# Kernel optimization log

Measured on AMD Instinct MI355X. Metric: run time of the kernel, lower is better.

Reference implementation:

```python
import jax, jax.numpy as jnp
import numpy as np

B = 8192
I = 1024
H = 1024


def _xavier(key, out_dim, in_dim):
    limit = float(np.sqrt(6.0 / (in_dim + out_dim)))
    return jax.random.uniform(key, (out_dim, in_dim), jnp.float32, -limit, limit)


def setup_inputs() -> dict:
    key = jax.random.key(0)
    ks = jax.random.split(key, 16)
    inp = {
        "x": jax.random.normal(ks[0], (B, I), jnp.float32),
        "h_prev": jax.random.normal(ks[1], (B, H), jnp.float32),
        "c_prev": jax.random.normal(ks[2], (B, H), jnp.float32),
        # input->hidden weights (hidden_size, input_size), hidden->hidden (hidden_size, hidden_size)
        "Wxi": _xavier(ks[3], H, I), "Whi": _xavier(ks[4], H, H),
        "Wxf": _xavier(ks[5], H, I), "Whf": _xavier(ks[6], H, H),
        "Wxc": _xavier(ks[7], H, I), "Whc": _xavier(ks[8], H, H),
        "Wxo": _xavier(ks[9], H, I), "Who": _xavier(ks[10], H, H),
        "bxi": jnp.zeros((H,), jnp.float32), "bhi": jnp.zeros((H,), jnp.float32),
        # forget-gate biases initialized to ones per _init_weights
        "bxf": jnp.ones((H,), jnp.float32), "bhf": jnp.ones((H,), jnp.float32),
        "bxc": jnp.zeros((H,), jnp.float32), "bhc": jnp.zeros((H,), jnp.float32),
        "bxo": jnp.zeros((H,), jnp.float32), "bho": jnp.zeros((H,), jnp.float32),
    }
    return inp


def reference(x, h_prev, c_prev,
              Wxi, Whi, Wxf, Whf, Wxc, Whc, Wxo, Who,
              bxi, bhi, bxf, bhf, bxc, bhc, bxo, bho):
    # Fuse the 8 small linears into two GEMMs: stack along the output (gate) axis.
    Wx = jnp.concatenate([Wxi, Wxf, Wxc, Wxo], axis=0)   # (4H, I)
    Wh = jnp.concatenate([Whi, Whf, Whc, Who], axis=0)   # (4H, H)
    bx = jnp.concatenate([bxi, bxf, bxc, bxo], axis=0)    # (4H,)
    bh = jnp.concatenate([bhi, bhf, bhc, bho], axis=0)    # (4H,)
    gates = x @ Wx.T + h_prev @ Wh.T + (bx + bh)           # (B, 4H)
    zi, zf, zc, zo = jnp.split(gates, 4, axis=1)
    i = jax.nn.sigmoid(zi)
    f = jax.nn.sigmoid(zf)
    g = jnp.tanh(zc)
    o = jax.nn.sigmoid(zo)
    c_new = f * c_prev + i * g
    h_new = o * jnp.tanh(c_new)
    return (h_new, c_new)
```

## Files before the change

### kernel.cpp

```cpp
#include <hip/hip_runtime.h>
#include <hip/hip_bf16.h>
#include <stdint.h>


#define B_DIM 8192
#define I_DIM 1024
#define H_DIM 1024
#define K_DIM 2048
#define N_DIM 4096
#define NKT   32

typedef short bf16x8 __attribute__((ext_vector_type(8)));
typedef float f32x4 __attribute__((ext_vector_type(4)));

__device__ __forceinline__ unsigned short f2bf(float f) {
  unsigned int u = __float_as_uint(f);
  u += 0x7FFFu + ((u >> 16) & 1u);
  return (unsigned short)(u >> 16);
}

__global__ void pack_AB_kernel(const float* __restrict__ x, const float* __restrict__ h,
                               const float* __restrict__ Wxi, const float* __restrict__ Whi,
                               const float* __restrict__ Wxf, const float* __restrict__ Whf,
                               const float* __restrict__ Wxc, const float* __restrict__ Whc,
                               const float* __restrict__ Wxo, const float* __restrict__ Who,
                               unsigned short* __restrict__ outA,
                               unsigned short* __restrict__ outB) {
  const int totalA = B_DIM * K_DIM / 8;
  const int total  = totalA + N_DIM * K_DIM / 8;
  for (int idx = blockIdx.x * blockDim.x + threadIdx.x; idx < total;
       idx += gridDim.x * blockDim.x) {
    const float* src;
    unsigned short* dst;
    if (idx < totalA) {
      int row = idx >> 8;
      int col = (idx & 255) * 8;
      src = (col < I_DIM) ? (x + (size_t)row * I_DIM + col)
                          : (h + (size_t)row * H_DIM + (col - I_DIM));
      dst = outA + (size_t)idx * 8;
    } else {
      int u2 = idx - totalA;
      int r = u2 >> 8;
      int k = (u2 & 255) * 8;
      int g = (r >> 4) & 3;
      int hh = ((r >> 6) << 4) | (r & 15);
      src = (k < I_DIM)
          ? ((g == 0 ? Wxi : g == 1 ? Wxf : g == 2 ? Wxc : Wxo) + (size_t)hh * I_DIM + k)
          : ((g == 0 ? Whi : g == 1 ? Whf : g == 2 ? Whc : Who) + (size_t)hh * H_DIM + (k - I_DIM));
      dst = outB + (size_t)u2 * 8;
    }
    const float4* s4 = (const float4*)src;
    float4 v0 = s4[0], v1 = s4[1];
    bf16x8 o;
    o[0] = f2bf(v0.x); o[1] = f2bf(v0.y); o[2] = f2bf(v0.z); o[3] = f2bf(v0.w);
    o[4] = f2bf(v1.x); o[5] = f2bf(v1.y); o[6] = f2bf(v1.z); o[7] = f2bf(v1.w);
    *(bf16x8*)dst = o;
  }
}


#define STAGE(gptr, slotoff, ktile) do {                                          \
    int _ktc = (ktile) < NKT ? (ktile) : (NKT - 1);                               \
    const unsigned short* _g = (gptr) + (size_t)_ktc * 64;                        \
    __builtin_amdgcn_global_load_lds(                                             \
        (const __attribute__((address_space(1))) void*)_g,                        \
        (__attribute__((address_space(3))) void*)(lds + (slotoff) + wid * 1024),  \
        16, 0, 0);                                                                \
    __builtin_amdgcn_global_load_lds(                                             \
        (const __attribute__((address_space(1))) void*)(_g + (size_t)64 * K_DIM), \
        (__attribute__((address_space(3))) void*)(lds + (slotoff) + 8192 + wid * 1024), \
        16, 0, 0);                                                                \
  } while (0)

#define MFMAP(MH, AR, BR)                                                         \
  _Pragma("unroll") for (int mf = 0; mf < 4; ++mf)                                \
  _Pragma("unroll") for (int nn = 0; nn < 4; ++nn)                                \
    acc[(MH)*4 + mf][nn] = __builtin_amdgcn_mfma_f32_16x16x32_bf16(               \
        AR[mf], BR[nn], acc[(MH)*4 + mf][nn], 0, 0, 0)

#define RD_AQ(DST, MH, KOFF, BO)                                                  \
  _Pragma("unroll") for (int mf = 0; mf < 4; ++mf)                                \
    DST[mf] = *(const bf16x8*)(ldsAr + (BO) + (MH)*8192 + mf * 2048 + (KOFF));

#define RD_BH(DST, KOFF, BO)                                                      \
  _Pragma("unroll") for (int nn = 0; nn < 4; ++nn)                                \
    DST[nn] = *(const bf16x8*)(ldsBr + (BO) + nn * 2048 + (KOFF));

#define KTILE(BUF, KT) do {                                                       \
    const int _bo = (BUF) * 32768;                                                \
    const int _bo1 = ((BUF) ^ 1) * 32768;                                         \
                                                                          \
    __builtin_amdgcn_s_setprio(1);                                                \
    MFMAP(0, AQa, BHa);                                                           \
    __builtin_amdgcn_s_setprio(0);                                                \
    RD_AQ(AQb, 1, rd0, _bo);                                                      \
    __builtin_amdgcn_s_barrier();                                                 \
                                                                          \
    __builtin_amdgcn_s_setprio(1);                                                \
    MFMAP(1, AQb, BHa);                                                           \
    __builtin_amdgcn_s_setprio(0);                                                \
    RD_BH(BHb, rd1, _bo);                                                         \
    RD_AQ(AQa, 0, rd1, _bo);                                                      \
    __builtin_amdgcn_s_barrier();                                                 \
                                                                          \
    __builtin_amdgcn_s_setprio(1);                                                \
    MFMAP(0, AQa, BHb);                                                           \
    __builtin_amdgcn_s_setprio(0);                                                \
    RD_AQ(AQb, 1, rd1, _bo);                                                      \
    STAGE(gB0p, 65536 + _bo, (KT) + 2);                                           \
    STAGE(gB1p, 65536 + _bo + 16384, (KT) + 2);                                   \
    asm volatile("s_waitcnt vmcnt(4)" ::: "memory");                              \
    __builtin_amdgcn_s_barrier();                                                 \
                                                                          \
    __builtin_amdgcn_s_setprio(1);                                                \
    MFMAP(1, AQb, BHb);                                                           \
    __builtin_amdgcn_s_setprio(0);                                                \
    RD_AQ(AQa, 0, rd0, _bo1);                                                     \
    RD_BH(BHa, rd0, _bo1);                                                        \
    STAGE(gA0p, _bo, (KT) + 2);                                                   \
    STAGE(gA1p, _bo + 16384, (KT) + 2);                                           \
    __builtin_amdgcn_s_barrier();                                                 \
  } while (0)

__launch_bounds__(512, 2)
__global__ void lstm_gemm_kernel(const unsigned short* __restrict__ A,
                                 const unsigned short* __restrict__ Bp,
                                 const float* __restrict__ c_prev,
                                 const float* __restrict__ bxi, const float* __restrict__ bhi,
                                 const float* __restrict__ bxf, const float* __restrict__ bhf,
                                 const float* __restrict__ bxc, const float* __restrict__ bhc,
                                 const float* __restrict__ bxo, const float* __restrict__ bho,
                                 float* __restrict__ out) {
  __shared__ __align__(16) char lds[131072];

  const int nwg = gridDim.x;
  int bid = blockIdx.x;
  int q = nwg >> 3;
  int wg = (bid & 7) * q + (bid >> 3);
  int bm = wg >> 4;
  int bn = wg & 15;

  int tid = threadIdx.x;
  int lane = tid & 63;
  int wid = tid >> 6;
  int wm = wid >> 2;
  int wn = wid & 3;

  int srow = lane >> 3;
  int schunk = (lane & 7) ^ srow;
  const unsigned short* gA0p = A  + (size_t)(bm * 256 + wid * 8 + srow) * K_DIM + schunk * 8;
  const unsigned short* gA1p = gA0p + (size_t)128 * K_DIM;
  const unsigned short* gB0p = Bp + (size_t)(bn * 256 + wid * 8 + srow) * K_DIM + schunk * 8;
  const unsigned short* gB1p = gB0p + (size_t)128 * K_DIM;

  int c15 = lane & 15;
  int kl = lane >> 4;
  const char* ldsAr = lds + wm * 16384 + c15 * 128;
  const char* ldsBr = lds + 65536 + (wn >> 1) * 16384 + ((wn & 1) * 64 + c15) * 128;
  int rd0 = ((kl) ^ (lane & 7)) << 4;
  int rd1 = ((4 | kl) ^ (lane & 7)) << 4;

  f32x4 acc[8][4];
  f32x4 zero = {0.f, 0.f, 0.f, 0.f};
#pragma unroll
  for (int m = 0; m < 8; ++m)
#pragma unroll
    for (int n = 0; n < 4; ++n) acc[m][n] = zero;

  bf16x8 AQa[4], AQb[4];
  bf16x8 BHa[4], BHb[4];

  STAGE(gA0p, 0, 0);
  STAGE(gA1p, 16384, 0);
  STAGE(gB0p, 65536, 0);
  STAGE(gB1p, 65536 + 16384, 0);
  STAGE(gA0p, 32768, 1);
  STAGE(gA1p, 32768 + 16384, 1);
  STAGE(gB0p, 65536 + 32768, 1);
  STAGE(gB1p, 65536 + 32768 + 16384, 1);
  asm volatile("s_waitcnt vmcnt(8)" ::: "memory");
  __builtin_amdgcn_s_barrier();
  RD_AQ(AQa, 0, rd0, 0);
  RD_BH(BHa, rd0, 0);

#pragma unroll 1
  for (int kt = 0; kt < NKT; kt += 2) {
    KTILE(0, kt);
    KTILE(1, kt + 1);
  }

  int h = (bn * 4 + wn) * 16 + c15;
  float bi = bxi[h] + bhi[h];
  float bf_ = bxf[h] + bhf[h];
  float bc = bxc[h] + bhc[h];
  float bo = bxo[h] + bho[h];
  int row0 = bm * 256 + wm * 128 + kl * 4;
#pragma unroll
  for (int mi = 0; mi < 8; ++mi) {
#pragma unroll
    for (int j = 0; j < 4; ++j) {
      int r = row0 + mi * 16 + j;
      size_t off = (size_t)r * H_DIM + h;
      float zi = acc[mi][0][j] + bi;
      float zf = acc[mi][1][j] + bf_;
      float zc = acc[mi][2][j] + bc;
      float zo = acc[mi][3][j] + bo;
      float ig = 1.f / (1.f + __expf(-zi));
      float fg = 1.f / (1.f + __expf(-zf));
      float e2 = __expf(-2.f * zc);
      float gg = (1.f - e2) / (1.f + e2);
      float og = 1.f / (1.f + __expf(-zo));
      float cp = c_prev[off];
      float cn = fg * cp + ig * gg;
      float e2c = __expf(-2.f * cn);
      float th = (1.f - e2c) / (1.f + e2c);
      out[off] = og * th;
      out[(size_t)B_DIM * H_DIM + off] = cn;
    }
  }
}

extern "C" void kernel_launch(void* const* d_in, const int* in_sizes, int n_in,
                              void* d_out, int out_size, void* d_ws, size_t ws_size,
                              hipStream_t stream) {
  const float* x      = (const float*)d_in[0];
  const float* h_prev = (const float*)d_in[1];
  const float* c_prev = (const float*)d_in[2];
  const float* Wxi = (const float*)d_in[3];
  const float* Whi = (const float*)d_in[4];
  const float* Wxf = (const float*)d_in[5];
  const float* Whf = (const float*)d_in[6];
  const float* Wxc = (const float*)d_in[7];
  const float* Whc = (const float*)d_in[8];
  const float* Wxo = (const float*)d_in[9];
  const float* Who = (const float*)d_in[10];
  const float* bxi = (const float*)d_in[11];
  const float* bhi = (const float*)d_in[12];
  const float* bxf = (const float*)d_in[13];
  const float* bhf = (const float*)d_in[14];
  const float* bxc = (const float*)d_in[15];
  const float* bhc = (const float*)d_in[16];
  const float* bxo = (const float*)d_in[17];
  const float* bho = (const float*)d_in[18];

  unsigned short* Abf = (unsigned short*)d_ws;
  unsigned short* Bbf = (unsigned short*)((char*)d_ws + (size_t)B_DIM * K_DIM * 2);

  pack_AB_kernel<<<2048, 256, 0, stream>>>(x, h_prev,
      Wxi, Whi, Wxf, Whf, Wxc, Whc, Wxo, Who, Abf, Bbf);
  lstm_gemm_kernel<<<512, 512, 0, stream>>>(Abf, Bbf, c_prev,
      bxi, bhi, bxf, bhf, bxc, bhc, bxo, bho, (float*)d_out);
}
```

Baseline: 152.1 us.

## Shrink GEMM workgroup tile to 256x128 with K=32 stages and 4 waves

Reworks the bf16 MFMA GEMM from 512-thread workgroups with 256x256 tiles and K-step 64 into 256-thread workgroups with 256x128 tiles and K-step 32. That cuts LDS use from 128KB to 48KB, doubles the grid to 1024 blocks, and uses a new swizzle and a simpler two-phase double-buffered schedule with sched_barriers. The goal is better occupancy and load balance across CUs and simpler LDS reads. In exchange, arithmetic intensity per tile drops, B-matrix reuse is halved, and twice as many K iterations add barrier overhead.

Result: slower. 178.3 us (+17.3%).

```diff
diff --git a/kernel.cpp b/kernel.cpp
--- a/kernel.cpp
+++ b/kernel.cpp
@@ -8,7 +8,7 @@
 #define H_DIM 1024
 #define K_DIM 2048
 #define N_DIM 4096
-#define NKT   32
+#define NKT   64
 
 typedef short bf16x8 __attribute__((ext_vector_type(8)));
 typedef float f32x4 __attribute__((ext_vector_type(4)));
@@ -59,17 +59,22 @@
 }
 
 
-#define STAGE(gptr, slotoff, ktile) do {                                          \
-    int _ktc = (ktile) < NKT ? (ktile) : (NKT - 1);                               \
-    const unsigned short* _g = (gptr) + (size_t)_ktc * 64;                        \
-    __builtin_amdgcn_global_load_lds(                                             \
-        (const __attribute__((address_space(1))) void*)_g,                        \
-        (__attribute__((address_space(3))) void*)(lds + (slotoff) + wid * 1024),  \
-        16, 0, 0);                                                                \
-    __builtin_amdgcn_global_load_lds(                                             \
-        (const __attribute__((address_space(1))) void*)(_g + (size_t)64 * K_DIM), \
-        (__attribute__((address_space(3))) void*)(lds + (slotoff) + 8192 + wid * 1024), \
-        16, 0, 0);                                                                \
+#define STAGE_A(BUF, KT) do {                                                     \
+    int _ktc = (KT) < NKT ? (KT) : (NKT - 1);                                     \
+    _Pragma("unroll") for (int i = 0; i < 4; ++i)                                 \
+      __builtin_amdgcn_global_load_lds(                                           \
+          (const __attribute__((address_space(1))) void*)(gAs + (size_t)i * 16 * K_DIM + (size_t)_ktc * 32), \
+          (__attribute__((address_space(3))) void*)(lds + (BUF) * 16384 + wid * 4096 + i * 1024), \
+          16, 0, 0);                                                              \
+  } while (0)
+
+#define STAGE_B(BUF, KT) do {                                                     \
+    int _ktc = (KT) < NKT ? (KT) : (NKT - 1);                                     \
+    _Pragma("unroll") for (int i = 0; i < 2; ++i)                                 \
+      __builtin_amdgcn_global_load_lds(                                           \
+          (const __attribute__((address_space(1))) void*)(gBs + (size_t)i * 16 * K_DIM + (size_t)_ktc * 32), \
+          (__attribute__((address_space(3))) void*)(lds + 32768 + (BUF) * 8192 + wid * 2048 + i * 1024), \
+          16, 0, 0);                                                              \
   } while (0)
 
 #define MFMAP(MH, AR, BR)                                                         \
@@ -78,51 +83,38 @@
     acc[(MH)*4 + mf][nn] = __builtin_amdgcn_mfma_f32_16x16x32_bf16(               \
         AR[mf], BR[nn], acc[(MH)*4 + mf][nn], 0, 0, 0)
 
-#define RD_AQ(DST, MH, KOFF, BO)                                                  \
+#define RD_AQ(DST, MH, BUF)                                                       \
   _Pragma("unroll") for (int mf = 0; mf < 4; ++mf)                                \
-    DST[mf] = *(const bf16x8*)(ldsAr + (BO) + (MH)*8192 + mf * 2048 + (KOFF));
-
-#define RD_BH(DST, KOFF, BO)                                                      \
+    DST[mf] = *(const bf16x8*)(ldsAr + (BUF) * 16384 + ((MH)*4 + mf) * 1024);
+
+#define RD_BQ(DST, BUF)                                                           \
   _Pragma("unroll") for (int nn = 0; nn < 4; ++nn)                                \
-    DST[nn] = *(const bf16x8*)(ldsBr + (BO) + nn * 2048 + (KOFF));
-
-#define KTILE(BUF, KT) do {                                                       \
-    const int _bo = (BUF) * 32768;                                                \
-    const int _bo1 = ((BUF) ^ 1) * 32768;                                         \
-                                                                          \
+    DST[nn] = *(const bf16x8*)(ldsBr + (BUF) * 8192 + nn * 1024);
+
+#define KTILE(BUF, KT, BQcur, BQnext) do {                                        \
+          \
     __builtin_amdgcn_s_setprio(1);                                                \
-    MFMAP(0, AQa, BHa);                                                           \
+    MFMAP(0, AQa, BQcur);                                                         \
     __builtin_amdgcn_s_setprio(0);                                                \
-    RD_AQ(AQb, 1, rd0, _bo);                                                      \
+    STAGE_A((BUF), (KT) + 2);                                                     \
+    STAGE_B((BUF), (KT) + 2);                                                     \
+    asm volatile("s_waitcnt vmcnt(6)" ::: "memory");                              \
+    __builtin_amdgcn_sched_barrier(0);                                            \
     __builtin_amdgcn_s_barrier();                                                 \
-                                                                          \
+    __builtin_amdgcn_sched_barrier(0);                                            \
+          \
     __builtin_amdgcn_s_setprio(1);                                                \
-    MFMAP(1, AQb, BHa);                                                           \
+    MFMAP(1, AQb, BQcur);                                                         \
     __builtin_amdgcn_s_setprio(0);                                                \
-    RD_BH(BHb, rd1, _bo);                                                         \
-    RD_AQ(AQa, 0, rd1, _bo);                                                      \
+    RD_AQ(AQa, 0, (BUF) ^ 1);                                                     \
+    RD_AQ(AQb, 1, (BUF) ^ 1);                                                     \
+    RD_BQ(BQnext, (BUF) ^ 1);                                                     \
+    __builtin_amdgcn_sched_barrier(0);                                            \
     __builtin_amdgcn_s_barrier();                                                 \
-                                                                          \
-    __builtin_amdgcn_s_setprio(1);                                                \
-    MFMAP(0, AQa, BHb);                                                           \
-    __builtin_amdgcn_s_setprio(0);                                                \
-    RD_AQ(AQb, 1, rd1, _bo);                                                      \
-    STAGE(gB0p, 65536 + _bo, (KT) + 2);                                           \
-    STAGE(gB1p, 65536 + _bo + 16384, (KT) + 2);                                   \
-    asm volatile("s_waitcnt vmcnt(4)" ::: "memory");                              \
-    __builtin_amdgcn_s_barrier();                                                 \
-                                                                          \
-    __builtin_amdgcn_s_setprio(1);                                                \
-    MFMAP(1, AQb, BHb);                                                           \
-    __builtin_amdgcn_s_setprio(0);                                                \
-    RD_AQ(AQa, 0, rd0, _bo1);                                                     \
-    RD_BH(BHa, rd0, _bo1);                                                        \
-    STAGE(gA0p, _bo, (KT) + 2);                                                   \
-    STAGE(gA1p, _bo + 16384, (KT) + 2);                                           \
-    __builtin_amdgcn_s_barrier();                                                 \
+    __builtin_amdgcn_sched_barrier(0);                                            \
   } while (0)
 
-__launch_bounds__(512, 2)
+__launch_bounds__(256, 2)
 __global__ void lstm_gemm_kernel(const unsigned short* __restrict__ A,
                                  const unsigned short* __restrict__ Bp,
                                  const float* __restrict__ c_prev,
@@ -131,34 +123,30 @@
                                  const float* __restrict__ bxc, const float* __restrict__ bhc,
                                  const float* __restrict__ bxo, const float* __restrict__ bho,
                                  float* __restrict__ out) {
-  __shared__ __align__(16) char lds[131072];
+  __shared__ __align__(16) char lds[49152];
 
   const int nwg = gridDim.x;
   int bid = blockIdx.x;
   int q = nwg >> 3;
   int wg = (bid & 7) * q + (bid >> 3);
-  int bm = wg >> 4;
-  int bn = wg & 15;
+  int bm = wg >> 5;
+  int bn = wg & 31;
 
   int tid = threadIdx.x;
   int lane = tid & 63;
   int wid = tid >> 6;
-  int wm = wid >> 2;
-  int wn = wid & 3;
-
-  int srow = lane >> 3;
-  int schunk = (lane & 7) ^ srow;
-  const unsigned short* gA0p = A  + (size_t)(bm * 256 + wid * 8 + srow) * K_DIM + schunk * 8;
-  const unsigned short* gA1p = gA0p + (size_t)128 * K_DIM;
-  const unsigned short* gB0p = Bp + (size_t)(bn * 256 + wid * 8 + srow) * K_DIM + schunk * 8;
-  const unsigned short* gB1p = gB0p + (size_t)128 * K_DIM;
+  int wm = wid >> 1;
+  int wn = wid & 1;
+
+  int swc = (lane & 3) ^ ((lane >> 3) & 3);
+  const unsigned short* gAs = A  + (size_t)(bm * 256 + wid * 64 + (lane >> 2)) * K_DIM + swc * 8;
+  const unsigned short* gBs = Bp + (size_t)(bn * 128 + wid * 32 + (lane >> 2)) * K_DIM + swc * 8;
 
   int c15 = lane & 15;
   int kl = lane >> 4;
-  const char* ldsAr = lds + wm * 16384 + c15 * 128;
-  const char* ldsBr = lds + 65536 + (wn >> 1) * 16384 + ((wn & 1) * 64 + c15) * 128;
-  int rd0 = ((kl) ^ (lane & 7)) << 4;
-  int rd1 = ((4 | kl) ^ (lane & 7)) << 4;
+  int rdsw = ((kl ^ ((c15 >> 1) & 3)) << 4);
+  const char* ldsAr = lds + wm * 8192 + c15 * 64 + rdsw;
+  const char* ldsBr = lds + 32768 + wn * 4096 + c15 * 64 + rdsw;
 
   f32x4 acc[8][4];
   f32x4 zero = {0.f, 0.f, 0.f, 0.f};
@@ -168,28 +156,29 @@
     for (int n = 0; n < 4; ++n) acc[m][n] = zero;
 
   bf16x8 AQa[4], AQb[4];
-  bf16x8 BHa[4], BHb[4];
-
-  STAGE(gA0p, 0, 0);
-  STAGE(gA1p, 16384, 0);
-  STAGE(gB0p, 65536, 0);
-  STAGE(gB1p, 65536 + 16384, 0);
-  STAGE(gA0p, 32768, 1);
-  STAGE(gA1p, 32768 + 16384, 1);
-  STAGE(gB0p, 65536 + 32768, 1);
-  STAGE(gB1p, 65536 + 32768 + 16384, 1);
-  asm volatile("s_waitcnt vmcnt(8)" ::: "memory");
+  bf16x8 BQa[4], BQb[4];
+
+  STAGE_A(0, 0);
+  STAGE_B(0, 0);
+  STAGE_A(1, 1);
+  STAGE_B(1, 1);
+  asm volatile("s_waitcnt vmcnt(6)" ::: "memory");
   __builtin_amdgcn_s_barrier();
-  RD_AQ(AQa, 0, rd0, 0);
-  RD_BH(BHa, rd0, 0);
+  __builtin_amdgcn_sched_barrier(0);
+  RD_AQ(AQa, 0, 0);
+  RD_AQ(AQb, 1, 0);
+  RD_BQ(BQa, 0);
+  __builtin_amdgcn_sched_barrier(0);
+  __builtin_amdgcn_s_barrier();
+  __builtin_amdgcn_sched_barrier(0);
 
 #pragma unroll 1
   for (int kt = 0; kt < NKT; kt += 2) {
-    KTILE(0, kt);
-    KTILE(1, kt + 1);
+    KTILE(0, kt, BQa, BQb);
+    KTILE(1, kt + 1, BQb, BQa);
   }
 
-  int h = (bn * 4 + wn) * 16 + c15;
+  int h = (bn * 2 + wn) * 16 + c15;
   float bi = bxi[h] + bhi[h];
   float bf_ = bxf[h] + bhf[h];
   float bc = bxc[h] + bhc[h];
@@ -248,6 +237,6 @@
 
   pack_AB_kernel<<<2048, 256, 0, stream>>>(x, h_prev,
       Wxi, Whi, Wxf, Whf, Wxc, Whc, Wxo, Who, Abf, Bbf);
-  lstm_gemm_kernel<<<512, 512, 0, stream>>>(Abf, Bbf, c_prev,
+  lstm_gemm_kernel<<<1024, 256, 0, stream>>>(Abf, Bbf, c_prev,
       bxi, bhi, bxf, bhf, bxc, bhc, bxo, bho, (float*)d_out);
 }
```
